# Performance work log

Hardware: AMD Instinct MI355X
Metric: run time of the kernel (lower is better)

Reference implementation:

```python
import jax, jax.numpy as jnp
import numpy as np

N_NODES = 150000
N_EDGES = 4800000
IN_DIM, HID_DIM, OUT_DIM = 1433, 16, 7


def setup_inputs() -> dict:
    key = jax.random.key(0)
    ks = jax.random.split(key, 8)
    features = jax.random.normal(ks[0], (N_NODES, IN_DIM), dtype=jnp.float32)
    edge_src = jax.random.randint(ks[1], (N_EDGES,), 0, N_NODES, dtype=jnp.int32)
    edge_dst = jax.random.randint(ks[2], (N_EDGES,), 0, N_NODES, dtype=jnp.int32)
    adj_vals = jax.random.uniform(ks[3], (N_EDGES,), dtype=jnp.float32)
    W1 = jax.random.normal(ks[4], (IN_DIM, HID_DIM), dtype=jnp.float32) * (1.0 / np.sqrt(IN_DIM))
    b1 = jnp.zeros((HID_DIM,), dtype=jnp.float32)
    W2 = jax.random.normal(ks[5], (HID_DIM, OUT_DIM), dtype=jnp.float32) * (1.0 / np.sqrt(HID_DIM))
    b2 = jnp.zeros((OUT_DIM,), dtype=jnp.float32)
    return {"features": features, "edge_src": edge_src, "edge_dst": edge_dst,
            "adj_vals": adj_vals, "W1": W1, "b1": b1, "W2": W2, "b2": b2}


def _gcn_layer(x, edge_src, edge_dst, adj_vals, W, b):
    # h = A_hat @ (x @ W) + b ; dense transform first since in_dim >= out_dim
    xw = x @ W                                   # [N, d_out]
    msg = adj_vals[:, None] * xw[edge_src]       # [E, d_out] gather
    agg = jax.ops.segment_sum(msg, edge_dst, num_segments=x.shape[0])  # scatter-add
    return agg + b


def reference(features, edge_src, edge_dst, adj_vals, W1, b1, W2, b2):
    h1 = jax.nn.relu(_gcn_layer(features, edge_src, edge_dst, adj_vals, W1, b1))
    # dropout in original forward is a no-op (result discarded) -> omitted
    h2 = _gcn_layer(h1, edge_src, edge_dst, adj_vals, W2, b2)
    return jax.nn.log_softmax(h2, axis=1)
```

## Files before the change

### kernel.cpp

```cpp
#include <hip/hip_runtime.h>
#include <float.h>
#include <stdint.h>

#define IN_DIM 1433
#define HID 16
#define OUTD 7

#define KC 32
#define GROWS 64
#define NT ((IN_DIM + KC - 1) / KC)
#define KLAST (IN_DIM - (NT - 1) * KC)

#define AS1 __attribute__((address_space(1)))
#define AS3 __attribute__((address_space(3)))

__global__ __launch_bounds__(256, 8) void gemm1_kernel(
    const float* __restrict__ feat, const float* __restrict__ W1,
    float* __restrict__ xw1, int N)
{
    __shared__ float xs[2][GROWS * KC];
    const int t = threadIdx.x;
    const int lane = t & 63;
    const int w = t >> 6;
    const int row0 = blockIdx.x * GROWS;
    const long maxElem = (long)N * IN_DIM - 1;

    const int r  = t & 63;
    const int rb = r & 7;
    const int q4 = __builtin_amdgcn_readfirstlane(w) * 4;

    float acc[4] = {0.f, 0.f, 0.f, 0.f};

    auto stage = [&](int buf, int k0) {
#pragma unroll
        for (int i = 0; i < 8; ++i) {
            const int ri = (i * 4 + w) * 2 + (lane >> 5);
            const int cs = lane & 31;
            const int gcol = (cs & 3) | (((cs >> 2) ^ (ri & 7)) << 2);
            long elem = (long)(row0 + ri) * IN_DIM + k0 + gcol;
            if (elem > maxElem) elem = maxElem;
            __builtin_amdgcn_global_load_lds(
                (const AS1 void*)(feat + elem),
                (AS3 void*)(&xs[buf][(i * 4 + w) * 64]), 4, 0, 0);
        }
    };

#define COMPUTE(buf, k0v, KMAX)                                              \
    {                                                                        \
        const float* xrow = &xs[buf][r * KC];                                \
        _Pragma("unroll")                                                    \
        for (int b = 0; b < ((KMAX) >> 2); ++b) {                            \
            const float4 xv = *(const float4*)&xrow[((b ^ rb) << 2)];        \
            const float* wk = W1 + (size_t)((k0v) + 4 * b) * HID + q4;       \
            const float4 w0 = *(const float4*)(wk);                          \
            const float4 w1 = *(const float4*)(wk + HID);                    \
            const float4 w2 = *(const float4*)(wk + 2 * HID);                \
            const float4 w3 = *(const float4*)(wk + 3 * HID);                \
            acc[0] += xv.x * w0.x; acc[1] += xv.x * w0.y;                    \
            acc[2] += xv.x * w0.z; acc[3] += xv.x * w0.w;                    \
            acc[0] += xv.y * w1.x; acc[1] += xv.y * w1.y;                    \
            acc[2] += xv.y * w1.z; acc[3] += xv.y * w1.w;                    \
            acc[0] += xv.z * w2.x; acc[1] += xv.z * w2.y;                    \
            acc[2] += xv.z * w2.z; acc[3] += xv.z * w2.w;                    \
            acc[0] += xv.w * w3.x; acc[1] += xv.w * w3.y;                    \
            acc[2] += xv.w * w3.z; acc[3] += xv.w * w3.w;                    \
        }                                                                    \
        if ((KMAX) & 3) {                     \
            const int b = (KMAX) >> 2;                                       \
            const float4 xv = *(const float4*)&xrow[((b ^ rb) << 2)];        \
            const float* wk = W1 + (size_t)((k0v) + 4 * b) * HID + q4;       \
            const float4 w0 = *(const float4*)(wk);                          \
            acc[0] += xv.x * w0.x; acc[1] += xv.x * w0.y;                    \
            acc[2] += xv.x * w0.z; acc[3] += xv.x * w0.w;                    \
        }                                                                    \
    }

    stage(0, 0);
    __syncthreads();
    for (int it = 0; it < NT - 1; ++it) {
        stage((it & 1) ^ 1, (it + 1) * KC);
        COMPUTE(it & 1, it * KC, KC);
        __syncthreads();
    }
    COMPUTE((NT - 1) & 1, (NT - 1) * KC, KLAST);
#undef COMPUTE

    const int grow = row0 + r;
    if (grow < N)
        *(float4*)(xw1 + (size_t)grow * HID + q4) =
            make_float4(acc[0], acc[1], acc[2], acc[3]);
}

__global__ __launch_bounds__(256) void hist_kernel(
    const int* __restrict__ dst, int* __restrict__ cnt, int E)
{
    const int e = blockIdx.x * 256 + threadIdx.x;
    if (e < E) atomicAdd(&cnt[dst[e]], 1);
}

__global__ __launch_bounds__(256) void scan1_kernel(
    const int* __restrict__ cnt, int* __restrict__ offs,
    int* __restrict__ bsum, int N)
{
    __shared__ int lds[256];
    const int t = threadIdx.x, b = blockIdx.x;
    const int base = b * 1024 + t * 4;
    int c0 = 0, c1 = 0, c2 = 0, c3 = 0;
    if (base + 0 < N) c0 = cnt[base + 0];
    if (base + 1 < N) c1 = cnt[base + 1];
    if (base + 2 < N) c2 = cnt[base + 2];
    if (base + 3 < N) c3 = cnt[base + 3];
    const int s = c0 + c1 + c2 + c3;
    lds[t] = s;
    __syncthreads();
    for (int off = 1; off < 256; off <<= 1) {
        int v = (t >= off) ? lds[t - off] : 0;
        __syncthreads();
        lds[t] += v;
        __syncthreads();
    }
    const int excl = lds[t] - s;
    if (t == 255) bsum[b] = lds[255];
    int run = excl;
    if (base + 0 < N) { offs[base + 0] = run; run += c0; }
    if (base + 1 < N) { offs[base + 1] = run; run += c1; }
    if (base + 2 < N) { offs[base + 2] = run; run += c2; }
    if (base + 3 < N) { offs[base + 3] = run; run += c3; }
}

__global__ __launch_bounds__(256) void scan2_kernel(
    const int* __restrict__ bsum, int* __restrict__ bbase, int NB)
{
    __shared__ int lds[256];
    const int t = threadIdx.x;
    const int v = (t < NB) ? bsum[t] : 0;
    lds[t] = v;
    __syncthreads();
    for (int off = 1; off < 256; off <<= 1) {
        int u = (t >= off) ? lds[t - off] : 0;
        __syncthreads();
        lds[t] += u;
        __syncthreads();
    }
    bbase[t] = lds[t] - v;
}

__global__ __launch_bounds__(256) void scan3_kernel(
    int* __restrict__ offs, int* __restrict__ cursor,
    const int* __restrict__ bbase, int N, int E)
{
    const int t = threadIdx.x, b = blockIdx.x;
    const int add = bbase[b];
    const int base = b * 1024 + t * 4;
#pragma unroll
    for (int i = 0; i < 4; ++i) {
        const int idx = base + i;
        if (idx < N) {
            const int v = offs[idx] + add;
            offs[idx] = v;
            cursor[idx] = v;
        }
    }
    if (b == 0 && t == 0) offs[N] = E;
}

__global__ __launch_bounds__(256) void fill_kernel(
    const int* __restrict__ src, const int* __restrict__ dst,
    const float* __restrict__ a, int* __restrict__ cursor,
    uint2* __restrict__ pairs, int E)
{
    const int e = blockIdx.x * 256 + threadIdx.x;
    if (e >= E) return;
    const int d = dst[e];
    const int pos = atomicAdd(&cursor[d], 1);
    pairs[pos] = make_uint2((unsigned)src[e], __float_as_uint(a[e]));
}

__global__ __launch_bounds__(256) void gather1_kernel(
    const uint2* __restrict__ pairs, const int* __restrict__ offs,
    const float* __restrict__ xw1, const float* __restrict__ b1,
    const float* __restrict__ W2, float* __restrict__ xw2, int N)
{
    __shared__ float w2s[HID * OUTD];
    const int t = threadIdx.x;
    if (t < HID * OUTD) w2s[t] = W2[t];
    __syncthreads();
    const int lane = t & 63;
    const int r = blockIdx.x * 4 + (t >> 6);
    if (r >= N) return;
    const int g = lane >> 2;
    const int c = lane & 3;
    const int start = offs[r], end = offs[r + 1];
    float4 acc = make_float4(0.f, 0.f, 0.f, 0.f);
    int e = start + g;
    for (; e + 16 < end; e += 32) {
        const uint2 p0 = pairs[e];
        const uint2 p1 = pairs[e + 16];
        const float4 v0 = *(const float4*)(xw1 + (size_t)p0.x * HID + c * 4);
        const float4 v1 = *(const float4*)(xw1 + (size_t)p1.x * HID + c * 4);
        const float a0 = __uint_as_float(p0.y);
        const float a1 = __uint_as_float(p1.y);
        acc.x += a0 * v0.x + a1 * v1.x;
        acc.y += a0 * v0.y + a1 * v1.y;
        acc.z += a0 * v0.z + a1 * v1.z;
        acc.w += a0 * v0.w + a1 * v1.w;
    }
    if (e < end) {
        const uint2 p0 = pairs[e];
        const float4 v0 = *(const float4*)(xw1 + (size_t)p0.x * HID + c * 4);
        const float a0 = __uint_as_float(p0.y);
        acc.x += a0 * v0.x; acc.y += a0 * v0.y;
        acc.z += a0 * v0.z; acc.w += a0 * v0.w;
    }
#pragma unroll
    for (int m = 4; m < 64; m <<= 1) {
        acc.x += __shfl_xor(acc.x, m);
        acc.y += __shfl_xor(acc.y, m);
        acc.z += __shfl_xor(acc.z, m);
        acc.w += __shfl_xor(acc.w, m);
    }
    const float4 b1v = ((const float4*)b1)[c];
    float4 h;
    h.x = fmaxf(acc.x + b1v.x, 0.f);
    h.y = fmaxf(acc.y + b1v.y, 0.f);
    h.z = fmaxf(acc.z + b1v.z, 0.f);
    h.w = fmaxf(acc.w + b1v.w, 0.f);
    float hh[16];
#pragma unroll
    for (int cc = 0; cc < 4; ++cc) {
        hh[cc * 4 + 0] = __shfl(h.x, cc);
        hh[cc * 4 + 1] = __shfl(h.y, cc);
        hh[cc * 4 + 2] = __shfl(h.z, cc);
        hh[cc * 4 + 3] = __shfl(h.w, cc);
    }
    const int col = (lane & 7) < OUTD ? (lane & 7) : 0;
    float sacc = 0.f;
#pragma unroll
    for (int j = 0; j < HID; ++j) sacc += hh[j] * w2s[j * OUTD + col];
    if (lane < 8) xw2[(size_t)r * 8 + lane] = (lane < OUTD) ? sacc : 0.f;
}

__global__ __launch_bounds__(256) void gather2_kernel(
    const uint2* __restrict__ pairs, const int* __restrict__ offs,
    const float* __restrict__ xw2, const float* __restrict__ b2,
    float* __restrict__ out, int N)
{
    const int t = threadIdx.x;
    const int lane = t & 63;
    const int r = blockIdx.x * 4 + (t >> 6);
    if (r >= N) return;
    const int g = lane >> 1;
    const int c = lane & 1;
    const int start = offs[r], end = offs[r + 1];
    float4 acc = make_float4(0.f, 0.f, 0.f, 0.f);
    for (int e = start + g; e < end; e += 32) {
        const uint2 p = pairs[e];
        const float4 v = *(const float4*)(xw2 + (size_t)p.x * 8 + c * 4);
        const float a = __uint_as_float(p.y);
        acc.x += a * v.x; acc.y += a * v.y;
        acc.z += a * v.z; acc.w += a * v.w;
    }
#pragma unroll
    for (int m = 2; m < 64; m <<= 1) {
        acc.x += __shfl_xor(acc.x, m);
        acc.y += __shfl_xor(acc.y, m);
        acc.z += __shfl_xor(acc.z, m);
        acc.w += __shfl_xor(acc.w, m);
    }
    float4 x;
    if (c == 0) {
        const float4 b2v = *(const float4*)b2;
        x.x = acc.x + b2v.x; x.y = acc.y + b2v.y;
        x.z = acc.z + b2v.z; x.w = acc.w + b2v.w;
    } else {
        x.x = acc.x + b2[4]; x.y = acc.y + b2[5];
        x.z = acc.z + b2[6]; x.w = -FLT_MAX;
    }
    float mymax = fmaxf(fmaxf(x.x, x.y), x.z);
    if (c == 0) mymax = fmaxf(mymax, x.w);
    const float m = fmaxf(mymax, __shfl_xor(mymax, 1));
    float es = expf(x.x - m) + expf(x.y - m) + expf(x.z - m);
    if (c == 0) es += expf(x.w - m);
    const float s = es + __shfl_xor(es, 1);
    const float lg = logf(s);
    float* op = out + (size_t)r * OUTD;
    if (c == 0) {
        op[0] = x.x - m - lg; op[1] = x.y - m - lg;
        op[2] = x.z - m - lg; op[3] = x.w - m - lg;
    } else {
        op[4] = x.x - m - lg; op[5] = x.y - m - lg;
        op[6] = x.z - m - lg;
    }
}

extern "C" void kernel_launch(void* const* d_in, const int* in_sizes, int n_in,
                              void* d_out, int out_size, void* d_ws, size_t ws_size,
                              hipStream_t stream)
{
    const float* feat  = (const float*)d_in[0];
    const int*   esrc  = (const int*)d_in[1];
    const int*   edst  = (const int*)d_in[2];
    const float* avals = (const float*)d_in[3];
    const float* W1    = (const float*)d_in[4];
    const float* b1    = (const float*)d_in[5];
    const float* W2    = (const float*)d_in[6];
    const float* b2    = (const float*)d_in[7];
    float* out = (float*)d_out;

    const int N = in_sizes[0] / IN_DIM;
    const int E = in_sizes[1];
    const int NB = (N + 1023) / 1024;

    char* p = (char*)d_ws;
    float* xw1   = (float*)p; p += (size_t)N * HID * sizeof(float);
    float* xw2   = (float*)p; p += (size_t)N * 8 * sizeof(float);
    int*   cnt   = (int*)p;   p += (size_t)N * sizeof(int);
    int*   offs  = (int*)p;   p += (size_t)(N + 1) * sizeof(int);
    int*   cursor= (int*)p;   p += (size_t)N * sizeof(int);
    int*   bsum  = (int*)p;   p += 256 * sizeof(int);
    int*   bbase = (int*)p;   p += 256 * sizeof(int);
    p = (char*)(((uintptr_t)p + 15) & ~(uintptr_t)15);
    uint2* pairs = (uint2*)p;

    hipMemsetAsync(cnt, 0, (size_t)N * sizeof(int), stream);

    gemm1_kernel<<<(N + GROWS - 1) / GROWS, 256, 0, stream>>>(feat, W1, xw1, N);

    hist_kernel<<<(E + 255) / 256, 256, 0, stream>>>(edst, cnt, E);
    scan1_kernel<<<NB, 256, 0, stream>>>(cnt, offs, bsum, N);
    scan2_kernel<<<1, 256, 0, stream>>>(bsum, bbase, NB);
    scan3_kernel<<<NB, 256, 0, stream>>>(offs, cursor, bbase, N, E);
    fill_kernel<<<(E + 255) / 256, 256, 0, stream>>>(esrc, edst, avals, cursor, pairs, E);

    gather1_kernel<<<(N + 3) / 4, 256, 0, stream>>>(pairs, offs, xw1, b1, W2, xw2, N);
    gather2_kernel<<<(N + 3) / 4, 256, 0, stream>>>(pairs, offs, xw2, b2, out, N);
}
```

Before: 1.003 ms.

## Cache W1 in LDS and use persistent split-K GEMM blocks

The first-layer GEMM now runs as a persistent kernel: 256 blocks of 1024 threads, each loading all of W1 into shared memory once in a transposed layout and then looping over 64-row panels. The K dimension is tiled in chunks of 128 and split across four thread groups, whose partial sums are combined through shared memory. This removes the repeated global and cache reads of W1 and raises the bytes fetched per stage. In exchange it uses about 157 KB of LDS per block for a single resident block per CU, and adds extra barriers for the split-K reduction.

Measured after the change: 1.070 ms. +6.7%, slower.

```diff
diff --git a/kernel.cpp b/kernel.cpp
--- a/kernel.cpp
+++ b/kernel.cpp
@@ -6,89 +6,122 @@
 #define HID 16
 #define OUTD 7
 
-#define KC 32
-#define GROWS 64
-#define NT ((IN_DIM + KC - 1) / KC)
-#define KLAST (IN_DIM - (NT - 1) * KC)
+#define BR 64
+#define KT 128
+#define NTI 12
+#define KLASTI 25
+#define WLN (IN_DIM * HID)
 
 #define AS1 __attribute__((address_space(1)))
 #define AS3 __attribute__((address_space(3)))
 
-__global__ __launch_bounds__(256, 8) void gemm1_kernel(
+__global__ __launch_bounds__(1024, 1) void gemm1_kernel(
     const float* __restrict__ feat, const float* __restrict__ W1,
-    float* __restrict__ xw1, int N)
-{
-    __shared__ float xs[2][GROWS * KC];
+    float* __restrict__ xw1, int N, int NPAN)
+{
+    __shared__ float wl[WLN];
+    __shared__ float xs[2][BR * KT];
     const int t = threadIdx.x;
     const int lane = t & 63;
     const int w = t >> 6;
-    const int row0 = blockIdx.x * GROWS;
+
+    for (int i = t; i < WLN / 4; i += 1024) {
+        const float4 v = ((const float4*)W1)[i];
+        const int k = i >> 2;
+        const int q = i & 3;
+        float* d = wl + q * (IN_DIM * 4) + k * 4;
+        d[0] = v.x; d[1] = v.y; d[2] = v.z; d[3] = v.w;
+    }
+    __syncthreads();
+
+    const int r   = t & 63;
+    const int rx8 = r & 7;
+    const int q   = (t >> 6) & 3;
+    const int h   = t >> 8;
     const long maxElem = (long)N * IN_DIM - 1;
-
-    const int r  = t & 63;
-    const int rb = r & 7;
-    const int q4 = __builtin_amdgcn_readfirstlane(w) * 4;
-
-    float acc[4] = {0.f, 0.f, 0.f, 0.f};
-
-    auto stage = [&](int buf, int k0) {
-#pragma unroll
-        for (int i = 0; i < 8; ++i) {
-            const int ri = (i * 4 + w) * 2 + (lane >> 5);
-            const int cs = lane & 31;
-            const int gcol = (cs & 3) | (((cs >> 2) ^ (ri & 7)) << 2);
-            long elem = (long)(row0 + ri) * IN_DIM + k0 + gcol;
-            if (elem > maxElem) elem = maxElem;
-            __builtin_amdgcn_global_load_lds(
-                (const AS1 void*)(feat + elem),
-                (AS3 void*)(&xs[buf][(i * 4 + w) * 64]), 4, 0, 0);
+    const float* __restrict__ wq = wl + q * (IN_DIM * 4);
+
+    for (int pan = blockIdx.x; pan < NPAN; pan += gridDim.x) {
+        const int row0 = pan * BR;
+        float acc0 = 0.f, acc1 = 0.f, acc2 = 0.f, acc3 = 0.f;
+
+        auto stage = [&](int buf, int k0) {
+#pragma unroll
+            for (int i = 0; i < 8; ++i) {
+                const int ri   = w * 4 + (i >> 1);
+                const int half = i & 1;
+                const int fl   = half * 64 + lane;
+                const int b    = fl >> 2, e = fl & 3;
+                const int gcol = (((b & ~7) | ((b & 7) ^ (ri & 7))) << 2) | e;
+                long elem = (long)(row0 + ri) * IN_DIM + k0 + gcol;
+                if (elem > maxElem) elem = maxElem;
+                __builtin_amdgcn_global_load_lds(
+                    (const AS1 void*)(feat + elem),
+                    (AS3 void*)(&xs[buf][ri * KT + half * 64]), 4, 0, 0);
+            }
+        };
+
+        auto compute = [&](int buf, int k0, int klen) {
+            const int kb = h * 32;
+            int kl = klen - kb; if (kl > 32) kl = 32; if (kl < 0) kl = 0;
+            const float* xrow = &xs[buf][r * KT];
+#pragma unroll 8
+            for (int kk = 0; kk + 4 <= kl; kk += 4) {
+                const int bk = (kb + kk) >> 2;
+                const int sl = (bk & ~7) | ((bk & 7) ^ rx8);
+                const float4 xv = *(const float4*)&xrow[sl << 2];
+                const float* wp = wq + (size_t)(k0 + kb + kk) * 4;
+                const float4 w0 = *(const float4*)(wp);
+                const float4 w1 = *(const float4*)(wp + 4);
+                const float4 w2 = *(const float4*)(wp + 8);
+                const float4 w3 = *(const float4*)(wp + 12);
+                acc0 += xv.x * w0.x; acc1 += xv.x * w0.y;
+                acc2 += xv.x * w0.z; acc3 += xv.x * w0.w;
+                acc0 += xv.y * w1.x; acc1 += xv.y * w1.y;
+                acc2 += xv.y * w1.z; acc3 += xv.y * w1.w;
+                acc0 += xv.z * w2.x; acc1 += xv.z * w2.y;
+                acc2 += xv.z * w2.z; acc3 += xv.z * w2.w;
+                acc0 += xv.w * w3.x; acc1 += xv.w * w3.y;
+                acc2 += xv.w * w3.z; acc3 += xv.w * w3.w;
+            }
+            for (int kk = kl & ~3; kk < kl; ++kk) {
+                const int k = kb + kk;
+                const int bk = k >> 2;
+                const int sl = (bk & ~7) | ((bk & 7) ^ rx8);
+                const float x = xrow[(sl << 2) | (k & 3)];
+                const float* wp = wq + (size_t)(k0 + k) * 4;
+                acc0 += x * wp[0]; acc1 += x * wp[1];
+                acc2 += x * wp[2]; acc3 += x * wp[3];
+            }
+        };
+
+        stage(0, 0);
+        __syncthreads();
+        for (int it = 0; it < NTI - 1; ++it) {
+            stage((it + 1) & 1, (it + 1) * KT);
+            compute(it & 1, it * KT, KT);
+            __syncthreads();
         }
-    };
-
-#define COMPUTE(buf, k0v, KMAX)                                              \
-    {                                                                        \
-        const float* xrow = &xs[buf][r * KC];                                \
-        _Pragma("unroll")                                                    \
-        for (int b = 0; b < ((KMAX) >> 2); ++b) {                            \
-            const float4 xv = *(const float4*)&xrow[((b ^ rb) << 2)];        \
-            const float* wk = W1 + (size_t)((k0v) + 4 * b) * HID + q4;       \
-            const float4 w0 = *(const float4*)(wk);                          \
-            const float4 w1 = *(const float4*)(wk + HID);                    \
-            const float4 w2 = *(const float4*)(wk + 2 * HID);                \
-            const float4 w3 = *(const float4*)(wk + 3 * HID);                \
-            acc[0] += xv.x * w0.x; acc[1] += xv.x * w0.y;                    \
-            acc[2] += xv.x * w0.z; acc[3] += xv.x * w0.w;                    \
-            acc[0] += xv.y * w1.x; acc[1] += xv.y * w1.y;                    \
-            acc[2] += xv.y * w1.z; acc[3] += xv.y * w1.w;                    \
-            acc[0] += xv.z * w2.x; acc[1] += xv.z * w2.y;                    \
-            acc[2] += xv.z * w2.z; acc[3] += xv.z * w2.w;                    \
-            acc[0] += xv.w * w3.x; acc[1] += xv.w * w3.y;                    \
-            acc[2] += xv.w * w3.z; acc[3] += xv.w * w3.w;                    \
-        }                                                                    \
-        if ((KMAX) & 3) {                     \
-            const int b = (KMAX) >> 2;                                       \
-            const float4 xv = *(const float4*)&xrow[((b ^ rb) << 2)];        \
-            const float* wk = W1 + (size_t)((k0v) + 4 * b) * HID + q4;       \
-            const float4 w0 = *(const float4*)(wk);                          \
-            acc[0] += xv.x * w0.x; acc[1] += xv.x * w0.y;                    \
-            acc[2] += xv.x * w0.z; acc[3] += xv.x * w0.w;                    \
-        }                                                                    \
-    }
-
-    stage(0, 0);
-    __syncthreads();
-    for (int it = 0; it < NT - 1; ++it) {
-        stage((it & 1) ^ 1, (it + 1) * KC);
-        COMPUTE(it & 1, it * KC, KC);
-        __syncthreads();
-    }
-    COMPUTE((NT - 1) & 1, (NT - 1) * KC, KLAST);
-#undef COMPUTE
-
-    const int grow = row0 + r;
-    if (grow < N)
-        *(float4*)(xw1 + (size_t)grow * HID + q4) =
-            make_float4(acc[0], acc[1], acc[2], acc[3]);
+        compute((NTI - 1) & 1, (NTI - 1) * KT, KLASTI);
+
+        if (h) {
+            float* s = &xs[0][((h - 1) * 256 + (t & 255)) * 4];
+            s[0] = acc0; s[1] = acc1; s[2] = acc2; s[3] = acc3;
+        }
+        __syncthreads();
+        if (h == 0) {
+#pragma unroll
+            for (int u = 0; u < 3; ++u) {
+                const float* s = &xs[0][(u * 256 + t) * 4];
+                acc0 += s[0]; acc1 += s[1]; acc2 += s[2]; acc3 += s[3];
+            }
+            const int grow = row0 + r;
+            if (grow < N)
+                *(float4*)(xw1 + (size_t)grow * HID + q * 4) =
+                    make_float4(acc0, acc1, acc2, acc3);
+        }
+        __syncthreads();
+    }
 }
 
 __global__ __launch_bounds__(256) void hist_kernel(
@@ -220,18 +253,18 @@
         acc.w += __shfl_xor(acc.w, m);
     }
     const float4 b1v = ((const float4*)b1)[c];
-    float4 h;
-    h.x = fmaxf(acc.x + b1v.x, 0.f);
-    h.y = fmaxf(acc.y + b1v.y, 0.f);
-    h.z = fmaxf(acc.z + b1v.z, 0.f);
-    h.w = fmaxf(acc.w + b1v.w, 0.f);
+    float4 hv;
+    hv.x = fmaxf(acc.x + b1v.x, 0.f);
+    hv.y = fmaxf(acc.y + b1v.y, 0.f);
+    hv.z = fmaxf(acc.z + b1v.z, 0.f);
+    hv.w = fmaxf(acc.w + b1v.w, 0.f);
     float hh[16];
 #pragma unroll
     for (int cc = 0; cc < 4; ++cc) {
-        hh[cc * 4 + 0] = __shfl(h.x, cc);
-        hh[cc * 4 + 1] = __shfl(h.y, cc);
-        hh[cc * 4 + 2] = __shfl(h.z, cc);
-        hh[cc * 4 + 3] = __shfl(h.w, cc);
+        hh[cc * 4 + 0] = __shfl(hv.x, cc);
+        hh[cc * 4 + 1] = __shfl(hv.y, cc);
+        hh[cc * 4 + 2] = __shfl(hv.z, cc);
+        hh[cc * 4 + 3] = __shfl(hv.w, cc);
     }
     const int col = (lane & 7) < OUTD ? (lane & 7) : 0;
     float sacc = 0.f;
@@ -310,6 +343,7 @@
     const int N = in_sizes[0] / IN_DIM;
     const int E = in_sizes[1];
     const int NB = (N + 1023) / 1024;
+    const int NPAN = (N + BR - 1) / BR;
 
     char* p = (char*)d_ws;
     float* xw1   = (float*)p; p += (size_t)N * HID * sizeof(float);
@@ -324,7 +358,7 @@
 
     hipMemsetAsync(cnt, 0, (size_t)N * sizeof(int), stream);
 
-    gemm1_kernel<<<(N + GROWS - 1) / GROWS, 256, 0, stream>>>(feat, W1, xw1, N);
+    gemm1_kernel<<<256, 1024, 0, stream>>>(feat, W1, xw1, N, NPAN);
 
     hist_kernel<<<(E + 255) / 256, 256, 0, stream>>>(edst, cnt, E);
     scan1_kernel<<<NB, 256, 0, stream>>>(cnt, offs, bsum, N);
```

## Triple-buffer gemm1 LDS staging with vmcnt waits instead of full syncthreads

Applied to the files above, without the earlier changes.

The gemm1 feature staging moves from double to triple buffering. Each tile now waits with s_waitcnt vmcnt(8) plus a raw s_barrier, so one tile's async global_load_lds stays in flight while the next is computed. Per-row staging addresses are also hoisted into a precomputed ebase array. Costs are a third LDS buffer, hardcoded NT/KLAST constants, and lowering launch_bounds occupancy from 8 to 4 waves per SIMD.

Result: slower. 1.181 ms (+17.8%).

```diff
diff --git a/kernel.cpp b/kernel.cpp
--- a/kernel.cpp
+++ b/kernel.cpp
@@ -8,17 +8,17 @@
 
 #define KC 32
 #define GROWS 64
-#define NT ((IN_DIM + KC - 1) / KC)
-#define KLAST (IN_DIM - (NT - 1) * KC)
+#define NT 45
+#define KLAST 25
 
 #define AS1 __attribute__((address_space(1)))
 #define AS3 __attribute__((address_space(3)))
 
-__global__ __launch_bounds__(256, 8) void gemm1_kernel(
+__global__ __launch_bounds__(256, 4) void gemm1_kernel(
     const float* __restrict__ feat, const float* __restrict__ W1,
     float* __restrict__ xw1, int N)
 {
-    __shared__ float xs[2][GROWS * KC];
+    __shared__ float xs[3][GROWS * KC];
     const int t = threadIdx.x;
     const int lane = t & 63;
     const int w = t >> 6;
@@ -29,15 +29,21 @@
     const int rb = r & 7;
     const int q4 = __builtin_amdgcn_readfirstlane(w) * 4;
 
+    long ebase[8];
+#pragma unroll
+    for (int i = 0; i < 8; ++i) {
+        const int ri = (i * 4 + w) * 2 + (lane >> 5);
+        const int cs = lane & 31;
+        const int gcol = (cs & 3) | (((cs >> 2) ^ (ri & 7)) << 2);
+        ebase[i] = (long)(row0 + ri) * IN_DIM + gcol;
+    }
+
     float acc[4] = {0.f, 0.f, 0.f, 0.f};
 
     auto stage = [&](int buf, int k0) {
 #pragma unroll
         for (int i = 0; i < 8; ++i) {
-            const int ri = (i * 4 + w) * 2 + (lane >> 5);
-            const int cs = lane & 31;
-            const int gcol = (cs & 3) | (((cs >> 2) ^ (ri & 7)) << 2);
-            long elem = (long)(row0 + ri) * IN_DIM + k0 + gcol;
+            long elem = ebase[i] + k0;
             if (elem > maxElem) elem = maxElem;
             __builtin_amdgcn_global_load_lds(
                 (const AS1 void*)(feat + elem),
@@ -75,15 +81,28 @@
         }                                                                    \
     }
 
+#define WAITBAR(Nimm)                                                        \
+    asm volatile("s_waitcnt vmcnt(" #Nimm ")" ::: "memory");                 \
+    __builtin_amdgcn_sched_barrier(0);                                       \
+    __builtin_amdgcn_s_barrier();                                            \
+    __builtin_amdgcn_sched_barrier(0);
+
     stage(0, 0);
-    __syncthreads();
-    for (int it = 0; it < NT - 1; ++it) {
-        stage((it & 1) ^ 1, (it + 1) * KC);
-        COMPUTE(it & 1, it * KC, KC);
-        __syncthreads();
-    }
-    COMPUTE((NT - 1) & 1, (NT - 1) * KC, KLAST);
+    stage(1, KC);
+    for (int g = 0; g < 13; ++g) {
+        const int k0 = g * (3 * KC);
+        WAITBAR(8); stage(2, k0 + 2 * KC); COMPUTE(0, k0, KC);
+        WAITBAR(8); stage(0, k0 + 3 * KC); COMPUTE(1, k0 + KC, KC);
+        WAITBAR(8); stage(1, k0 + 4 * KC); COMPUTE(2, k0 + 2 * KC, KC);
+    }
+    WAITBAR(8); stage(2, 41 * KC); COMPUTE(0, 39 * KC, KC);
+    WAITBAR(8); stage(0, 42 * KC); COMPUTE(1, 40 * KC, KC);
+    WAITBAR(8); stage(1, 43 * KC); COMPUTE(2, 41 * KC, KC);
+    WAITBAR(8); stage(2, 44 * KC); COMPUTE(0, 42 * KC, KC);
+    WAITBAR(8);                    COMPUTE(1, 43 * KC, KC);
+    WAITBAR(0);                    COMPUTE(2, 44 * KC, KLAST);
 #undef COMPUTE
+#undef WAITBAR
 
     const int grow = row0 + r;
     if (grow < N)
@@ -220,18 +239,18 @@
         acc.w += __shfl_xor(acc.w, m);
     }
     const float4 b1v = ((const float4*)b1)[c];
-    float4 h;
-    h.x = fmaxf(acc.x + b1v.x, 0.f);
-    h.y = fmaxf(acc.y + b1v.y, 0.f);
-    h.z = fmaxf(acc.z + b1v.z, 0.f);
-    h.w = fmaxf(acc.w + b1v.w, 0.f);
+    float4 hv;
+    hv.x = fmaxf(acc.x + b1v.x, 0.f);
+    hv.y = fmaxf(acc.y + b1v.y, 0.f);
+    hv.z = fmaxf(acc.z + b1v.z, 0.f);
+    hv.w = fmaxf(acc.w + b1v.w, 0.f);
     float hh[16];
 #pragma unroll
     for (int cc = 0; cc < 4; ++cc) {
-        hh[cc * 4 + 0] = __shfl(h.x, cc);
-        hh[cc * 4 + 1] = __shfl(h.y, cc);
-        hh[cc * 4 + 2] = __shfl(h.z, cc);
-        hh[cc * 4 + 3] = __shfl(h.w, cc);
+        hh[cc * 4 + 0] = __shfl(hv.x, cc);
+        hh[cc * 4 + 1] = __shfl(hv.y, cc);
+        hh[cc * 4 + 2] = __shfl(hv.z, cc);
+        hh[cc * 4 + 3] = __shfl(hv.w, cc);
     }
     const int col = (lane & 7) < OUTD ? (lane & 7) : 0;
     float sacc = 0.f;
```
